# Kernel tuning notes

Hardware: AMD Instinct MI355X
Metric: run time of the kernel (lower is better)

The kernel has to match this reference:

```python
import jax, jax.numpy as jnp
import numpy as np

B, N, M = 8, 1024, 64          # graphs, ops/graph, machines/graph
OPF, MF = 16, 8                # raw feature dims
H, D, L = 8, 64, 3             # heads, head dim, HGT layers
F = H * D                      # 512 = hidden_dim * num_heads
KC = 8                         # compatible machines per op
NOP, NM = B * N, B * M
EPS = 1e-5


def _graph_ln(x, w, b):
    # PyG LayerNorm(mode='graph') with batch=None: scalar mean/std over the whole tensor
    x = x - x.mean()
    return x / (x.std() + EPS) * w + b


def _seg_softmax(a, idx, n):
    amax = jax.ops.segment_max(a, idx, num_segments=n)
    amax = jnp.where(jnp.isfinite(amax), amax, 0.0)
    ex = jnp.exp(a - amax[idx])
    s = jax.ops.segment_sum(ex, idx, num_segments=n)
    return ex / (s[idx] + 1e-16)


def _forward(op_x, machine_x, W_emb_op, b_emb_op, W_emb_m, b_emb_m,
             opn_w, opn_b, mn_w, mn_b, Wk, bk, Wq, bq, Wv, bv,
             A_rel, M_rel, p_rel, W_out, b_out, skip, ln_w, ln_b,
             ei_precedes, ei_canproc, ei_compat):
    x_op = _graph_ln(op_x @ W_emb_op + b_emb_op, opn_w, opn_b)
    x_m = _graph_ln(machine_x @ W_emb_m + b_emb_m, mn_w, mn_b)
    s0, d0 = ei_precedes   # op -> op
    s1, d1 = ei_canproc    # machine -> op
    s2, d2 = ei_compat     # op -> machine
    scale = 1.0 / jnp.sqrt(jnp.float32(D))
    for l in range(L):
        k_op = (x_op @ Wk[l, 0] + bk[l, 0]).reshape(NOP, H, D)
        q_op = (x_op @ Wq[l, 0] + bq[l, 0]).reshape(NOP, H, D)
        v_op = (x_op @ Wv[l, 0] + bv[l, 0]).reshape(NOP, H, D)
        k_m = (x_m @ Wk[l, 1] + bk[l, 1]).reshape(NM, H, D)
        q_m = (x_m @ Wq[l, 1] + bq[l, 1]).reshape(NM, H, D)
        v_m = (x_m @ Wv[l, 1] + bv[l, 1]).reshape(NM, H, D)
        # relation-specific per-head transforms (a_rel/m_rel of HGTConv)
        k0 = jnp.einsum('nhd,hde->nhe', k_op, A_rel[l, 0]); v0 = jnp.einsum('nhd,hde->nhe', v_op, M_rel[l, 0])
        k1 = jnp.einsum('nhd,hde->nhe', k_m, A_rel[l, 1]);  v1 = jnp.einsum('nhd,hde->nhe', v_m, M_rel[l, 1])
        k2 = jnp.einsum('nhd,hde->nhe', k_op, A_rel[l, 2]); v2 = jnp.einsum('nhd,hde->nhe', v_op, M_rel[l, 2])
        # attention into op nodes: joint softmax over both incoming edge types
        a0 = (q_op[d0] * k0[s0]).sum(-1) * p_rel[l, 0] * scale   # [E0,H]
        a1 = (q_op[d1] * k1[s1]).sum(-1) * p_rel[l, 1] * scale   # [E1,H]
        a_op = jnp.concatenate([a0, a1]); dd = jnp.concatenate([d0, d1])
        w = _seg_softmax(a_op, dd, NOP)
        msg = jnp.concatenate([v0[s0], v1[s1]]) * w[:, :, None]
        agg_op = jax.ops.segment_sum(msg, dd, num_segments=NOP).reshape(NOP, F)
        # attention into machine nodes
        a2 = (q_m[d2] * k2[s2]).sum(-1) * p_rel[l, 2] * scale
        w2 = _seg_softmax(a2, d2, NM)
        agg_m = jax.ops.segment_sum(v2[s2] * w2[:, :, None], d2, num_segments=NM).reshape(NM, F)
        # output projection + learned skip gate (HGTConv internals)
        o_op = jax.nn.gelu(agg_op, approximate=False) @ W_out[l, 0] + b_out[l, 0]
        o_m = jax.nn.gelu(agg_m, approximate=False) @ W_out[l, 1] + b_out[l, 1]
        g_op = jax.nn.sigmoid(skip[l, 0]); g_m = jax.nn.sigmoid(skip[l, 1])
        o_op = g_op * o_op + (1.0 - g_op) * x_op
        o_m = g_m * o_m + (1.0 - g_m) * x_m
        # wrapper residual + dropout(eval=identity) + graph layer norm
        x_op = _graph_ln(o_op + x_op, ln_w[l], ln_b[l])
        x_m = _graph_ln(o_m + x_m, ln_w[l], ln_b[l])
    fea_j = x_op.reshape(B, N, F)
    fea_m = x_m.reshape(B, M, F)
    return fea_j, fea_m, fea_j.mean(1, keepdims=True), fea_m.mean(1, keepdims=True)


def setup_inputs() -> dict:
    key = jax.random.key(0)
    ks = jax.random.split(key, 12)
    rng = np.random.default_rng(0)
    ids = np.arange(NOP).reshape(B, N)
    src0 = ids[:, :-1].ravel(); dst0 = ids[:, 1:].ravel()
    mach = rng.integers(0, M, size=(B, N, KC)) + (np.arange(B) * M)[:, None, None]
    ops = np.broadcast_to(ids[:, :, None], (B, N, KC))
    ei_precedes = jnp.asarray(np.stack([src0, dst0]), dtype=jnp.int32)
    ei_canproc = jnp.asarray(np.stack([mach.ravel(), ops.ravel()]), dtype=jnp.int32)
    ei_compat = jnp.asarray(np.stack([ops.ravel(), mach.ravel()]), dtype=jnp.int32)
    n = lambda k, sh, s=0.05: jax.random.normal(k, sh, dtype=jnp.float32) * s
    return dict(
        op_x=n(ks[0], (NOP, OPF), 1.0),
        machine_x=n(ks[1], (NM, MF), 1.0),
        W_emb_op=n(ks[2], (OPF, F)), b_emb_op=jnp.zeros((F,), jnp.float32),
        W_emb_m=n(ks[3], (MF, F)), b_emb_m=jnp.zeros((F,), jnp.float32),
        opn_w=jnp.ones((F,), jnp.float32), opn_b=jnp.zeros((F,), jnp.float32),
        mn_w=jnp.ones((F,), jnp.float32), mn_b=jnp.zeros((F,), jnp.float32),
        Wk=n(ks[4], (L, 2, F, F)), bk=jnp.zeros((L, 2, F), jnp.float32),
        Wq=n(ks[5], (L, 2, F, F)), bq=jnp.zeros((L, 2, F), jnp.float32),
        Wv=n(ks[6], (L, 2, F, F)), bv=jnp.zeros((L, 2, F), jnp.float32),
        A_rel=n(ks[7], (L, 3, H, D, D)), M_rel=n(ks[8], (L, 3, H, D, D)),
        p_rel=jnp.ones((L, 3, H), jnp.float32),
        W_out=n(ks[9], (L, 2, F, F)), b_out=jnp.zeros((L, 2, F), jnp.float32),
        skip=jnp.ones((L, 2), jnp.float32),
        ln_w=jnp.ones((L, F), jnp.float32), ln_b=jnp.zeros((L, F), jnp.float32),
        ei_precedes=ei_precedes, ei_canproc=ei_canproc, ei_compat=ei_compat,
    )


def reference(op_x, machine_x, W_emb_op, b_emb_op, W_emb_m, b_emb_m,
              opn_w, opn_b, mn_w, mn_b, Wk, bk, Wq, bq, Wv, bv,
              A_rel, M_rel, p_rel, W_out, b_out, skip, ln_w, ln_b,
              ei_precedes, ei_canproc, ei_compat):
    return _forward(op_x, machine_x, W_emb_op, b_emb_op, W_emb_m, b_emb_m,
                    opn_w, opn_b, mn_w, mn_b, Wk, bk, Wq, bq, Wv, bv,
                    A_rel, M_rel, p_rel, W_out, b_out, skip, ln_w, ln_b,
                    ei_precedes, ei_canproc, ei_compat)
```

## Files before the change

kernel.cpp:

```cpp
#include <hip/hip_runtime.h>

typedef unsigned short u16;
typedef __attribute__((ext_vector_type(4))) float floatx4;
typedef __attribute__((ext_vector_type(8))) short shortx8;
typedef __attribute__((ext_vector_type(4))) short shortx4;

#define NOPS 8192
#define NMS  512
#define CQ   2560
#define CM   1536
#define TOPC (NOPS*512)
#define TMC  (NMS*512)

__device__ __forceinline__ float bf2f(u16 u){ return __uint_as_float(((unsigned)u)<<16); }
__device__ __forceinline__ u16 f2bf(float f){
  unsigned u = __float_as_uint(f);
  u += 0x7FFFu + ((u>>16)&1u);
  return (u16)(u>>16);
}
__device__ __forceinline__ float wred(float v){
  #pragma unroll
  for (int o=32;o;o>>=1) v += __shfl_xor(v,o,64);
  return v;
}
__device__ __forceinline__ float geluf(float x){
  return 0.5f*x*(1.f+erff(x*0.70710678118654752f));
}
__device__ __forceinline__ void block_stat_out2(float s, float s2, float* pstat, int slot){
  __shared__ float sb[8];
  s = wred(s); s2 = wred(s2);
  int wv = threadIdx.x >> 6;
  if ((threadIdx.x & 63) == 0){ sb[wv*2] = s; sb[wv*2+1] = s2; }
  __syncthreads();
  if (threadIdx.x == 0){
    float a = 0.f, b = 0.f;
    int nw = blockDim.x >> 6;
    for (int i=0;i<nw;++i){ a += sb[i*2]; b += sb[i*2+1]; }
    pstat[slot*2]   = a;
    pstat[slot*2+1] = b;
  }
}

__global__ __launch_bounds__(256) void setup_all_k(
    const int* __restrict__ s1, float* __restrict__ Ct, float* __restrict__ Cn,
    const float* __restrict__ bq, float* bias_op, float* bias_m,
    const float* __restrict__ bk, const float* __restrict__ bv,
    const float* __restrict__ Ar, const float* __restrict__ Mr,
    const float* __restrict__ Wout, const float* __restrict__ Wq,
    u16* __restrict__ Wout_t, u16* __restrict__ Wc_op_t, u16* __restrict__ Wc_m_t,
    const float* __restrict__ Wk, const float* __restrict__ Wv,
    const float* __restrict__ Xop, const float* __restrict__ Wop, const float* __restrict__ bop,
    float* __restrict__ Yop, u16* __restrict__ Yop_bf,
    const float* __restrict__ Xm, const float* __restrict__ Wm, const float* __restrict__ bm_,
    float* __restrict__ Ym, u16* __restrict__ Ym_bf,
    float* pstat, float* pstat_m){
  __shared__ __align__(16) char smem[27648];
  int bid = blockIdx.x;
  int tid = threadIdx.x;
  if (bid < 1152){
    int eb = bid;
    const float *X, *W, *bias; float *Y, *ps; u16* Yb; int K, total4, nb, lb;
    if (eb < 1024){ X=Xop; W=Wop; bias=bop; Y=Yop; Yb=Yop_bf; ps=pstat;   K=16; total4=TOPC/4; nb=1024; lb=eb; }
    else          { X=Xm;  W=Wm;  bias=bm_; Y=Ym;  Yb=Ym_bf;  ps=pstat_m; K=8;  total4=TMC/4;  nb=128;  lb=eb-1024; }
    float s = 0.f, s2 = 0.f;
    for (int idx = lb*256 + tid; idx < total4; idx += nb*256){
      int n = idx >> 7, f4 = idx & 127;
      floatx4 v = *(const floatx4*)(bias + f4*4);
      const float* xrow = X + n*K;
      for (int c=0;c<K;++c){
        float xc = xrow[c];
        floatx4 wv = *(const floatx4*)(W + c*512 + f4*4);
        #pragma unroll
        for (int e=0;e<4;++e) v[e] += xc*wv[e];
      }
      shortx4 sv;
      #pragma unroll
      for (int e=0;e<4;++e){ sv[e] = (short)f2bf(v[e]); s += v[e]; s2 += v[e]*v[e]; }
      *(floatx4*)(Y + (size_t)idx*4) = v;
      *(shortx4*)(Yb + (size_t)idx*4) = sv;
    }
    block_stat_out2(s, s2, ps, lb);
  } else if (bid < 1920){
    u16 (*t)[65] = (u16(*)[65])smem;
    int id2 = bid - 1152;
    int g = id2 >> 6; int rem = id2 & 63;
    int kb = (rem >> 3) * 64, nb = (rem & 7) * 64;
    const float* s; u16* d;
    if (g < 6){
      s = Wout + (size_t)g*262144;
      d = Wout_t + (size_t)g*262144;
    } else {
      int blk = g - 6; int l = blk >> 1, side = blk & 1;
      s = Wq + (size_t)blk*262144;
      d = side ? (Wc_m_t + (size_t)l*CM*512) : (Wc_op_t + (size_t)l*CQ*512);
    }
    int tx = tid & 63, ty4 = tid >> 6;
    #pragma unroll 4
    for (int p=0;p<16;++p){
      int k = ty4 + p*4;
      t[k][tx] = f2bf(s[(size_t)(kb+k)*512 + nb + tx]);
    }
    __syncthreads();
    #pragma unroll 4
    for (int p=0;p<16;++p){
      int n = ty4 + p*4;
      d[(size_t)(nb+n)*512 + kb + tx] = t[tx][n];
    }
  } else if (bid < 2496){
    u16* As = (u16*)smem;
    u16* Bs = As + 64*72;
    int id3 = bid - 1920;
    int gx = id3 >> 2;
    int cc0 = (id3 & 3) * 128;
    int l = gx/48; int rem = gx - l*48; int s = rem >> 3; int h = rem & 7;
    int side = (s < 4) ? 0 : 1;
    int r = (s < 4) ? (s+1) : (s-3);
    int useK = side==0 ? (s==0 || s==2) : (s==4);
    int rel  = side==0 ? ((s<2)?0:2) : 1;
    const float* W   = (useK ? Wk : Wv) + (size_t)(l*2+side)*262144;
    const float* Rel = (useK ? Ar : Mr) + ((size_t)(l*3+rel)*8 + h)*4096;
    int h64 = h*64;
    u16* Wt = side ? (Wc_m_t + (size_t)l*CM*512) : (Wc_op_t + (size_t)l*CQ*512);
    int rbase = r*512 + h64;
    int lane = tid & 63, wave = tid >> 6;
    {
      int d = tid >> 2, e0 = (tid & 3) * 16;
      #pragma unroll
      for (int j=0;j<16;++j) As[(e0+j)*72 + d] = f2bf(Rel[d*64 + e0 + j]);
    }
    {
      int ccl = tid >> 1, d0 = (tid & 1) * 32;
      const float* src = W + (size_t)(cc0+ccl)*512 + h64 + d0;
      #pragma unroll
      for (int j=0;j<32;j+=4){
        floatx4 v = *(const floatx4*)(src + j);
        shortx4 sv;
        #pragma unroll
        for (int e=0;e<4;++e) sv[e] = (short)f2bf(v[e]);
        *(shortx4*)(Bs + ccl*72 + d0 + j) = sv;
      }
    }
    __syncthreads();
    int wm = wave & 1, wn = wave >> 1;
    int mrow = lane & 15, quad = lane >> 4;
    floatx4 acc[2][4];
    #pragma unroll
    for (int a=0;a<2;++a)
      #pragma unroll
      for (int b=0;b<4;++b) acc[a][b] = (floatx4){0.f,0.f,0.f,0.f};
    #pragma unroll
    for (int ks=0; ks<2; ++ks){
      shortx8 af[2], bf[4];
      #pragma unroll
      for (int mt=0;mt<2;++mt) af[mt] = *(const shortx8*)(As + (wm*32 + mt*16 + mrow)*72 + ks*32 + quad*8);
      #pragma unroll
      for (int nt=0;nt<4;++nt) bf[nt] = *(const shortx8*)(Bs + (wn*64 + nt*16 + mrow)*72 + ks*32 + quad*8);
      #pragma unroll
      for (int mt=0;mt<2;++mt)
        #pragma unroll
        for (int nt=0;nt<4;++nt)
          acc[mt][nt] = __builtin_amdgcn_mfma_f32_16x16x32_bf16(af[mt], bf[nt], acc[mt][nt], 0, 0, 0);
    }
    #pragma unroll
    for (int mt=0;mt<2;++mt){
      #pragma unroll
      for (int nt=0;nt<4;++nt){
        int ccl = wn*64 + nt*16 + mrow;
        #pragma unroll
        for (int r2=0;r2<4;++r2){
          int e = wm*32 + mt*16 + quad*4 + r2;
          Wt[(size_t)(rbase + e)*512 + cc0 + ccl] = f2bf(acc[mt][nt][r2]);
        }
      }
    }
  } else if (bid < 4544){
    int idx = (bid-2496)*256 + tid;
    int n = idx >> 6, l = idx & 63;
    const int* row = s1 + n*8;
    int cnt = 0;
    #pragma unroll
    for (int j=0;j<8;++j) cnt += ((row[j] & 63) == l);
    float f = (float)cnt;
    Cn[(size_t)n*64 + l] = f;
    int b = n >> 10, nl = n & 1023;
    Ct[(size_t)((b<<6) + l)*1024 + nl] = f;
  } else if (bid < 4556){
    int i = (bid-4544)*256 + tid;
    int l = i >> 10, side = (i >> 9) & 1, f = i & 511;
    float v = bq[(l*2+side)*512 + f];
    if (side==0) bias_op[l*CQ + f] = v; else bias_m[l*CM + f] = v;
  } else {
    if (tid >= 64) return;
    int gx = bid - 4556; int e = tid;
    int l = gx/48; int rem = gx - l*48; int s = rem >> 3; int h = rem & 7;
    int side = (s < 4) ? 0 : 1;
    int r = (s < 4) ? (s+1) : (s-3);
    int useK = side==0 ? (s==0 || s==2) : (s==4);
    int rel  = side==0 ? ((s<2)?0:2) : 1;
    const float* bb  = (useK ? bk : bv) + (size_t)(l*2+side)*512 + h*64;
    const float* Rel = (useK ? Ar : Mr) + ((size_t)(l*3+rel)*8 + h)*4096;
    float acc = 0.f;
    for (int d=0; d<64; ++d) acc += bb[d]*Rel[d*64 + e];
    float* bias = side ? (bias_m + l*CM) : (bias_op + l*CQ);
    bias[r*512 + h*64 + e] = acc;
  }
}

__global__ __launch_bounds__(256) void foldk(u16* __restrict__ Wc_op_t, u16* __restrict__ Wc_m_t,
                                             float* __restrict__ bias_op, float* __restrict__ bias_m,
                                             float* __restrict__ u_op, float* __restrict__ u_m,
                                             const float* __restrict__ opn_w, const float* __restrict__ opn_b,
                                             const float* __restrict__ mn_w, const float* __restrict__ mn_b,
                                             const float* __restrict__ ln_w, const float* __restrict__ ln_b){
  int bid = blockIdx.x, tid = threadIdx.x;
  int rloc = tid >> 2, t = tid & 3;
  int side, l; u16* Wt; float* bias; float* u;
  if (bid < 120){
    int row = bid*64 + rloc; side = 0; l = row/2560; int j = row - l*2560;
    Wt = Wc_op_t + ((size_t)l*CQ + j)*512; bias = bias_op + l*CQ + j; u = u_op + l*CQ + j;
  } else {
    int row = (bid-120)*64 + rloc; side = 1; l = row/1536; int j = row - l*1536;
    Wt = Wc_m_t + ((size_t)l*CM + j)*512; bias = bias_m + l*CM + j; u = u_m + l*CM + j;
  }
  const float* w = side ? (l==0 ? mn_w : ln_w + (l-1)*512) : (l==0 ? opn_w : ln_w + (l-1)*512);
  const float* b = side ? (l==0 ? mn_b : ln_b + (l-1)*512) : (l==0 ? opn_b : ln_b + (l-1)*512);
  float up = 0.f, vp = 0.f;
  for (int k = t*128; k < t*128 + 128; k += 8){
    shortx8 wv = *(shortx8*)(Wt + k);
    #pragma unroll
    for (int e=0;e<8;++e){
      float x = bf2f((u16)wv[e]);
      float wk = w[k+e];
      up += wk*x; vp += b[k+e]*x;
      wv[e] = (short)f2bf(x*wk);
    }
    *(shortx8*)(Wt + k) = wv;
  }
  up += __shfl_xor(up,1,64); up += __shfl_xor(up,2,64);
  vp += __shfl_xor(vp,1,64); vp += __shfl_xor(vp,2,64);
  if (t == 0){ *u = up; *bias += vp; }
}

__global__ __launch_bounds__(256) void ln2_k(const float* __restrict__ src_op, float* __restrict__ dst_op,
                                             const float* __restrict__ w_op, const float* __restrict__ b_op,
                                             const float* __restrict__ src_m, float* __restrict__ dst_m,
                                             const float* __restrict__ w_m, const float* __restrict__ b_m,
                                             const float* __restrict__ pstat, const float* __restrict__ pstat_m,
                                             int nbo, int nbm){
  int bid = blockIdx.x;
  const float *src, *w, *b, *ps; float* dst; int total4, nb, lb, nblk; float inv_n;
  if (bid < 1024){ src=src_op; dst=dst_op; w=w_op; b=b_op; ps=pstat;
                   total4=TOPC/4; nb=1024; lb=bid; nblk=nbo; inv_n=1.f/TOPC; }
  else           { src=src_m;  dst=dst_m;  w=w_m;  b=b_m;  ps=pstat_m;
                   total4=TMC/4;  nb=128;  lb=bid-1024; nblk=nbm; inv_n=1.f/TMC; }
  __shared__ float sb[8];
  __shared__ float mr[2];
  float s = 0.f, s2 = 0.f;
  for (int i = threadIdx.x; i < nblk; i += 256){ s += ps[2*i]; s2 += ps[2*i+1]; }
  s = wred(s); s2 = wred(s2);
  int wv = threadIdx.x >> 6;
  if ((threadIdx.x & 63) == 0){ sb[wv*2] = s; sb[wv*2+1] = s2; }
  __syncthreads();
  if (threadIdx.x == 0){
    float a = 0.f, bsum = 0.f;
    for (int i=0;i<4;++i){ a += sb[i*2]; bsum += sb[i*2+1]; }
    float mean = a * inv_n;
    float var  = fmaxf(bsum * inv_n - mean*mean, 0.f);
    mr[0] = mean;
    mr[1] = 1.f/(sqrtf(var) + 1e-5f);
  }
  __syncthreads();
  float mean = mr[0], rinv = mr[1];
  const floatx4* s4 = (const floatx4*)src;
  floatx4* d4 = (floatx4*)dst;
  const floatx4* w4 = (const floatx4*)w;
  const floatx4* b4 = (const floatx4*)b;
  for (int i = lb*256 + threadIdx.x; i < total4; i += nb*256){
    int f = i & 127;
    floatx4 v = s4[i], wv2 = w4[f], bv = b4[f];
    #pragma unroll
    for (int e=0;e<4;++e) v[e] = (v[e]-mean)*rinv*wv2[e] + bv[e];
    d4[i] = v;
  }
}

__device__ __forceinline__ void gemm_gate_core(u16* As, u16* Bs, float* stb,
                                               const u16* __restrict__ A, const u16* __restrict__ Bt,
                                               const float* __restrict__ xr, const float* __restrict__ bo,
                                               const float* __restrict__ sk,
                                               const float* __restrict__ lnw, const float* __restrict__ lnb,
                                               const float* __restrict__ psr, int np, float inv_n,
                                               float* __restrict__ Y, u16* __restrict__ Ybf,
                                               float* pstat, int slot, int bx, int by){
  const int tid = threadIdx.x;
  const int lane = tid & 63, wave = tid >> 6;
  {
    float s = 0.f, s2 = 0.f;
    for (int i = tid; i < np; i += 256){ s += psr[2*i]; s2 += psr[2*i+1]; }
    s = wred(s); s2 = wred(s2);
    if (lane == 0){ stb[wave*2] = s; stb[wave*2+1] = s2; }
    __syncthreads();
    if (tid == 0){
      float a = 0.f, bb = 0.f;
      for (int i=0;i<4;++i){ a += stb[2*i]; bb += stb[2*i+1]; }
      float mean = a * inv_n;
      float var = fmaxf(bb * inv_n - mean*mean, 0.f);
      stb[8] = mean;
      stb[9] = 1.f/(sqrtf(var) + 1e-5f);
    }
    __syncthreads();
  }
  const float mean = stb[8], rinv = stb[9];
  const int bm = by * 128, bn = bx * 128;
  const int wm = wave & 1, wn = wave >> 1;
  const int mrow = lane & 15, quad = lane >> 4;
  const u16* Ab = A + (size_t)bm*512;
  const u16* Bb = Bt + (size_t)bn*512;
  floatx4 acc[4][4];
  #pragma unroll
  for (int a=0;a<4;++a)
    #pragma unroll
    for (int b=0;b<4;++b) acc[a][b] = (floatx4){0.f,0.f,0.f,0.f};
  const int r0 = tid >> 2, c0 = (tid & 3) * 8;
  const int r1 = (tid+256) >> 2, c1 = ((tid+256) & 3) * 8;
  const int lds0 = wave*512;
  const int lds1 = wave*512 + 2048;
  for (int k0 = 0; k0 < 512; k0 += 32){
    __builtin_amdgcn_global_load_lds((const __attribute__((address_space(1))) void*)(Ab + (size_t)r0*512 + k0 + c0),
                                     (__attribute__((address_space(3))) void*)(As + lds0), 16, 0, 0);
    __builtin_amdgcn_global_load_lds((const __attribute__((address_space(1))) void*)(Ab + (size_t)r1*512 + k0 + c1),
                                     (__attribute__((address_space(3))) void*)(As + lds1), 16, 0, 0);
    __builtin_amdgcn_global_load_lds((const __attribute__((address_space(1))) void*)(Bb + (size_t)r0*512 + k0 + c0),
                                     (__attribute__((address_space(3))) void*)(Bs + lds0), 16, 0, 0);
    __builtin_amdgcn_global_load_lds((const __attribute__((address_space(1))) void*)(Bb + (size_t)r1*512 + k0 + c1),
                                     (__attribute__((address_space(3))) void*)(Bs + lds1), 16, 0, 0);
    __syncthreads();
    shortx8 af[4], bf[4];
    #pragma unroll
    for (int mt=0;mt<4;++mt) af[mt] = *(const shortx8*)(As + (wm*64 + mt*16 + mrow)*32 + quad*8);
    #pragma unroll
    for (int nt=0;nt<4;++nt) bf[nt] = *(const shortx8*)(Bs + (wn*64 + nt*16 + mrow)*32 + quad*8);
    #pragma unroll
    for (int mt=0;mt<4;++mt)
      #pragma unroll
      for (int nt=0;nt<4;++nt)
        acc[mt][nt] = __builtin_amdgcn_mfma_f32_16x16x32_bf16(af[mt], bf[nt], acc[mt][nt], 0, 0, 0);
    __syncthreads();
  }
  float g = 1.f/(1.f+expf(-(*sk)));
  float s = 0.f, s2 = 0.f;
  #pragma unroll
  for (int mt=0;mt<4;++mt){
    #pragma unroll
    for (int nt=0;nt<4;++nt){
      int col = bn + wn*64 + nt*16 + mrow;
      float bval = bo[col];
      float lw = lnw[col]*rinv, lb = lnb[col];
      #pragma unroll
      for (int r2=0;r2<4;++r2){
        int row = bm + wm*64 + mt*16 + quad*4 + r2;
        float v = acc[mt][nt][r2] + bval;
        float xv = (xr[(size_t)row*512 + col] - mean)*lw + lb;
        float o = g*v + (2.f-g)*xv;
        Y[(size_t)row*512 + col] = o;
        Ybf[(size_t)row*512 + col] = f2bf(o);
        s += o; s2 += o*o;
      }
    }
  }
  block_stat_out2(s, s2, pstat, slot);
}
__global__ __launch_bounds__(256) void gemmgate2_k(
    const u16* A1, const u16* B1, const float* x1, const float* bo1, const float* sk1,
    const float* lnw1, const float* lnb1, float* Y1, u16* Yb1, float* ps1w, int nblk1,
    const u16* A2, const u16* B2, const float* x2, const float* bo2, const float* sk2,
    const float* lnw2, const float* lnb2, float* Y2, u16* Yb2, float* ps2w,
    const float* ps1r, int np1, const float* ps2r, int np2){
  __shared__ u16 As[128*32];
  __shared__ u16 Bs[128*32];
  __shared__ float stb[12];
  int id = blockIdx.x;
  if (id < nblk1)
    gemm_gate_core(As, Bs, stb, A1, B1, x1, bo1, sk1, lnw1, lnb1, ps1r, np1, 1.f/TOPC,
                   Y1, Yb1, ps1w, id, id % 4, id / 4);
  else {
    int j = id - nblk1;
    gemm_gate_core(As, Bs, stb, A2, B2, x2, bo2, sk2, lnw2, lnb2, ps2r, np2, 1.f/TMC,
                   Y2, Yb2, ps2w, j, j % 4, j / 4);
  }
}

__device__ __forceinline__ void stage_half8(const u16* __restrict__ src, int kc, u16* region, int tid){
  int wave = tid >> 6;
  #pragma unroll
  for (int j=0;j<2;++j){
    int idx = j*512 + tid;
    int row = idx >> 2, qp2 = idx & 3;
    int qs = qp2 ^ (((row >> 3) & 1) << 1);
    __builtin_amdgcn_global_load_lds(
      (const __attribute__((address_space(1))) void*)(src + (size_t)row*512 + kc + qs*8),
      (__attribute__((address_space(3))) void*)(region + (j*512 + wave*64)*8),
      16, 0, 0);
  }
}

#define MFMA_QUAD(MH) do { \
  __builtin_amdgcn_s_barrier(); \
  asm volatile("s_waitcnt lgkmcnt(0)" ::: "memory"); \
  __builtin_amdgcn_sched_barrier(0); \
  __builtin_amdgcn_s_setprio(1); \
  _Pragma("unroll") \
  for (int mt=0;mt<4;++mt){ \
    _Pragma("unroll") \
    for (int nt=0;nt<4;++nt) \
      acc[(MH)*4+mt][nt] = __builtin_amdgcn_mfma_f32_16x16x32_bf16(af[mt], bf[nt], acc[(MH)*4+mt][nt], 0, 0, 0); \
  } \
  __builtin_amdgcn_s_setprio(0); \
} while(0)

__global__ __launch_bounds__(512, 2) void gemm8_k(
    const u16* __restrict__ A1, const u16* __restrict__ B1, const float* __restrict__ bias1,
    const float* __restrict__ u1, u16* __restrict__ C1, int N1, int nbx1, int nblk1,
    const u16* __restrict__ A2, const u16* __restrict__ B2, const float* __restrict__ bias2p,
    const float* __restrict__ u2, u16* __restrict__ C2, int N2, int nbx2,
    const float* __restrict__ ps1, int np1, const float* __restrict__ ps2, int np2){
  extern __shared__ u16 lds[];
  float* statsh = (float*)(lds + 65536);
  int id = blockIdx.x;
  const u16 *A, *Bt; const float *bias, *uvec, *ps; u16* C; int N, bx, by, np; float inv_n;
  if (id < nblk1){
    int xcd = id & 7, loc = id >> 3;
    int wg = xcd * (nblk1 >> 3) + loc;
    A=A1; Bt=B1; bias=bias1; uvec=u1; C=C1; N=N1; bx=wg%nbx1; by=wg/nbx1;
    ps=ps1; np=np1; inv_n=1.f/TOPC;
  }
  else { int j=id-nblk1; A=A2; Bt=B2; bias=bias2p; uvec=u2; C=C2; N=N2; bx=j%nbx2; by=j/nbx2;
    ps=ps2; np=np2; inv_n=1.f/TMC; }
  const int tid = threadIdx.x, lane = tid & 63, wave = tid >> 6;
  {
    float s = 0.f, s2 = 0.f;
    for (int i = tid; i < np; i += 512){ s += ps[2*i]; s2 += ps[2*i+1]; }
    s = wred(s); s2 = wred(s2);
    if (lane == 0){ statsh[wave*2] = s; statsh[wave*2+1] = s2; }
    __syncthreads();
    if (tid == 0){
      float a = 0.f, bb = 0.f;
      for (int i=0;i<8;++i){ a += statsh[2*i]; bb += statsh[2*i+1]; }
      float mean = a * inv_n;
      float var = fmaxf(bb * inv_n - mean*mean, 0.f);
      statsh[16] = mean;
      statsh[17] = 1.f/(sqrtf(var) + 1e-5f);
    }
    __syncthreads();
  }
  const float mean = statsh[16], rinv = statsh[17];
  const int wm = wave & 1, wn = wave >> 1;
  const int mrow = lane & 15, quad = lane >> 4;
  const int qp = quad ^ ((mrow & 8) ? 2 : 0);
  const u16* Ab = A + (size_t)(by*256)*512;
  const u16* Bb = Bt + (size_t)(bx*256)*512;

  floatx4 acc[8][4];
  #pragma unroll
  for (int a=0;a<8;++a)
    #pragma unroll
    for (int b=0;b<4;++b) acc[a][b] = (floatx4){0.f,0.f,0.f,0.f};

  stage_half8(Ab, 0,  lds,          tid);
  stage_half8(Bb, 0,  lds + 16384,  tid);
  stage_half8(Ab, 32, lds + 8192,   tid);
  stage_half8(Bb, 32, lds + 24576,  tid);
  stage_half8(Ab, 64, lds + 32768,  tid);
  stage_half8(Bb, 64, lds + 49152,  tid);
  asm volatile("s_waitcnt vmcnt(8)" ::: "memory");
  __builtin_amdgcn_s_barrier();

  for (int t = 0; t < 8; ++t){
    const int s = t & 1;
    u16* Sbase = lds + s*32768;
    u16* Obase = lds + (s^1)*32768;
    const u16* a0 = Sbase + (wm*128 + mrow)*32 + qp*8;
    const u16* b0 = Sbase + 16384 + (wn*64 + mrow)*32 + qp*8;
    const int kc1 = ((t < 7) ? (t+1) : 7)*64 + 32;
    const int kc2 = ((t < 6) ? (t+2) : 7)*64;
    shortx8 af[4], bf[4];

    #pragma unroll
    for (int mt=0;mt<4;++mt) af[mt] = *(const shortx8*)(a0 + mt*512);
    #pragma unroll
    for (int nt=0;nt<4;++nt) bf[nt] = *(const shortx8*)(b0 + nt*512);
    stage_half8(Ab, kc1, Obase + 8192, tid);
    MFMA_QUAD(0);
    __builtin_amdgcn_s_barrier();

    #pragma unroll
    for (int mt=0;mt<4;++mt) af[mt] = *(const shortx8*)(a0 + 2048 + mt*512);
    stage_half8(Bb, kc1, Obase + 24576, tid);
    MFMA_QUAD(1);
    asm volatile("s_waitcnt vmcnt(8)" ::: "memory");
    __builtin_amdgcn_s_barrier();

    #pragma unroll
    for (int mt=0;mt<4;++mt) af[mt] = *(const shortx8*)(a0 + 8192 + mt*512);
    #pragma unroll
    for (int nt=0;nt<4;++nt) bf[nt] = *(const shortx8*)(b0 + 8192 + nt*512);
    stage_half8(Ab, kc2, Sbase, tid);
    MFMA_QUAD(0);
    __builtin_amdgcn_s_barrier();

    #pragma unroll
    for (int mt=0;mt<4;++mt) af[mt] = *(const shortx8*)(a0 + 8192 + 2048 + mt*512);
    stage_half8(Bb, kc2, Sbase + 16384, tid);
    MFMA_QUAD(1);
    asm volatile("s_waitcnt vmcnt(8)" ::: "memory");
    __builtin_amdgcn_s_barrier();
  }

  const float rm = rinv*mean;
  const int crow0 = by*256 + wm*128 + quad*4;
  const int ccol0 = bx*256 + wn*64 + mrow;
  float bv[4], uv[4];
  #pragma unroll
  for (int nt=0;nt<4;++nt){
    int col = ccol0 + nt*16;
    bv[nt] = bias[col];
    uv[nt] = uvec[col];
  }
  #pragma unroll
  for (int mh=0;mh<2;++mh){
    #pragma unroll
    for (int mt=0;mt<4;++mt){
      int row = crow0 + mh*64 + mt*16;
      #pragma unroll
      for (int nt=0;nt<4;++nt){
        int col = ccol0 + nt*16;
        #pragma unroll
        for (int r2=0;r2<4;++r2)
          C[(size_t)(row+r2)*N + col] = f2bf(rinv*acc[mh*4+mt][nt][r2] + bv[nt] - rm*uv[nt]);
      }
    }
  }
}

__global__ __launch_bounds__(256) void attn_k(const u16* __restrict__ qkv_op, const u16* __restrict__ qkv_m,
                                              const float* __restrict__ prel, const float* __restrict__ Cn,
                                              const float* __restrict__ Ct,
                                              u16* __restrict__ agg_op, u16* __restrict__ agg_m){
  __shared__ __align__(16) char smem[37376];
  int id = blockIdx.x;
  int tid = threadIdx.x, lane = tid & 63, wave = tid >> 6;
  int mrow = lane & 15, quad = lane >> 4;
  if (id < 256){
    u16* qs  = (u16*)smem;
    u16* ks  = (u16*)(smem + 2304);
    u16* vsT = (u16*)(smem + 11520);
    u16* Ps  = (u16*)(smem + 20736);
    float (*redv)[4][16] = (float(*)[4][16])(smem + 23040);
    int g = id & 3; int bh = id >> 2; int b = bh >> 3, h = bh & 7;
    int w = wave;
    float p2 = prel[16 + h] * 0.125f;
    if (tid < 128){
      int r = tid >> 3, cg = (tid & 7) * 8;
      *(shortx8*)(qs + r*72 + cg) = *(const shortx8*)(qkv_m + (size_t)(b*64 + g*16 + r)*CM + h*64 + cg);
    }
    const float* ctbase = Ct + (size_t)(b*64 + g*16 + mrow)*1024;
    float mold_m = -1e30f;
    float mold4[4] = {-1e30f,-1e30f,-1e30f,-1e30f};
    float L = 0.f;
    floatx4 O = (floatx4){0,0,0,0};
    for (int ch = 0; ch < 16; ++ch){
      int nb = ch*64;
      #pragma unroll
      for (int i=0;i<2;++i){
        int idx = i*256 + tid;
        int r = idx >> 3, cg = (idx & 7) * 8;
        *(shortx8*)(ks + r*72 + cg) =
          *(const shortx8*)(qkv_op + (size_t)(b*1024 + nb + r)*CQ + 1536 + h*64 + cg);
        shortx8 vv = *(const shortx8*)(qkv_op + (size_t)(b*1024 + nb + r)*CQ + 2048 + h*64 + cg);
        #pragma unroll
        for (int e=0;e<8;++e) vsT[(cg+e)*72 + r] = (u16)vv[e];
      }
      __syncthreads();
      floatx4 sa, cv;
      {
        floatx4 acc = (floatx4){0,0,0,0};
        #pragma unroll
        for (int kk=0; kk<2; ++kk){
          shortx8 af = *(const shortx8*)(ks + (w*16 + mrow)*72 + kk*32 + quad*8);
          shortx8 bf = *(const shortx8*)(qs + mrow*72 + kk*32 + quad*8);
          acc = __builtin_amdgcn_mfma_f32_16x16x32_bf16(af, bf, acc, 0, 0, 0);
        }
        int nloc = w*16 + quad*4;
        cv = *(const floatx4*)(ctbase + nb + nloc);
        #pragma unroll
        for (int r2=0;r2<4;++r2) acc[r2] *= p2;
        sa = acc;
      }
      float cm = -1e30f;
      #pragma unroll
      for (int r2=0;r2<4;++r2)
        if (cv[r2] > 0.f) cm = fmaxf(cm, sa[r2]);
      cm = fmaxf(cm, __shfl_xor(cm, 16, 64));
      cm = fmaxf(cm, __shfl_xor(cm, 32, 64));
      if (lane < 16) redv[0][w][lane] = cm;
      __syncthreads();
      float mnew_m = fmaxf(fmaxf(redv[0][0][mrow], redv[0][1][mrow]),
                           fmaxf(redv[0][2][mrow], redv[0][3][mrow]));
      mnew_m = fmaxf(mnew_m, mold_m);
      float sL = expf(mold_m - mnew_m);
      mold_m = mnew_m;
      float sO[4];
      #pragma unroll
      for (int r2=0;r2<4;++r2){
        int r = quad*4 + r2;
        float mn = fmaxf(fmaxf(redv[0][0][r], redv[0][1][r]),
                         fmaxf(redv[0][2][r], redv[0][3][r]));
        mn = fmaxf(mn, mold4[r2]);
        sO[r2] = expf(mold4[r2] - mn);
        mold4[r2] = mn;
      }
      float Lsum = 0.f;
      {
        int nloc = w*16 + quad*4;
        shortx4 pv;
        #pragma unroll
        for (int r2=0;r2<4;++r2){
          float e = (cv[r2] > 0.f) ? cv[r2]*expf(sa[r2] - mnew_m) : 0.f;
          Lsum += e;
          pv[r2] = (short)f2bf(e);
        }
        *(shortx4*)(Ps + mrow*72 + nloc) = pv;
      }
      L = L*sL + Lsum;
      __syncthreads();
      #pragma unroll
      for (int r2=0;r2<4;++r2) O[r2] *= sO[r2];
      #pragma unroll
      for (int kk=0; kk<2; ++kk){
        shortx8 af = *(const shortx8*)(Ps + mrow*72 + kk*32 + quad*8);
        shortx8 bf = *(const shortx8*)(vsT + (w*16 + mrow)*72 + kk*32 + quad*8);
        O = __builtin_amdgcn_mfma_f32_16x16x32_bf16(af, bf, O, 0, 0, 0);
      }
      __syncthreads();
    }
    L += __shfl_xor(L, 16, 64);
    L += __shfl_xor(L, 32, 64);
    if (lane < 16) redv[1][w][lane] = L;
    __syncthreads();
    #pragma unroll
    for (int r2=0;r2<4;++r2){
      int m = quad*4 + r2;
      float Ls = redv[1][0][m] + redv[1][1][m] + redv[1][2][m] + redv[1][3][m];
      float v = O[r2] / (Ls + 1e-16f);
      agg_m[(size_t)(b*64 + g*16 + m)*512 + h*64 + w*16 + mrow] = f2bf(geluf(v));
    }
  } else {
    u16* smem16 = (u16*)smem;
    u16* As = smem16;
    u16* Bs = smem16 + 4608;
    float* Sbuf = (float*)smem;
    u16* P   = smem16 + 9216;
    u16* v1T = smem16 + 13824;
    float* wpreS = (float*)(smem + 36864);
    float* linvS = (float*)(smem + 37120);
    int id2 = id - 256;
    int bh = id2 >> 4; int b = bh >> 3, h = bh & 7;
    int n0 = (id2 & 15) * 64;
    int wm = wave & 1, wn = wave >> 1;
    int srow = tid >> 2, scol = (tid & 3) * 16;
    float p1 = prel[8 + h] * 0.125f;
    {
      const u16* src = qkv_op + (size_t)(b*1024 + n0 + srow)*CQ + h*64 + scol;
      *(shortx8*)(As + srow*72 + scol)     = *(const shortx8*)(src);
      *(shortx8*)(As + srow*72 + scol + 8) = *(const shortx8*)(src + 8);
    }
    {
      const u16* src = qkv_m + (size_t)(b*64 + srow)*CM + 512 + h*64 + scol;
      *(shortx8*)(Bs + srow*72 + scol)     = *(const shortx8*)(src);
      *(shortx8*)(Bs + srow*72 + scol + 8) = *(const shortx8*)(src + 8);
    }
    {
      const u16* src = qkv_m + (size_t)(b*64 + srow)*CM + 1024 + h*64 + scol;
      shortx8 v0 = *(const shortx8*)(src);
      shortx8 v1 = *(const shortx8*)(src + 8);
      #pragma unroll
      for (int e=0;e<8;++e){ v1T[(scol+e)*72 + srow] = (u16)v0[e]; v1T[(scol+8+e)*72 + srow] = (u16)v1[e]; }
    }
    __syncthreads();
    floatx4 acc[2][2];
    #pragma unroll
    for (int a=0;a<2;++a){ acc[a][0] = (floatx4){0,0,0,0}; acc[a][1] = (floatx4){0,0,0,0}; }
    #pragma unroll
    for (int ks=0; ks<2; ++ks){
      shortx8 af[2], bf[2];
      #pragma unroll
      for (int mt=0;mt<2;++mt) af[mt] = *(const shortx8*)(As + (wm*32 + mt*16 + mrow)*72 + ks*32 + quad*8);
      #pragma unroll
      for (int nt=0;nt<2;++nt) bf[nt] = *(const shortx8*)(Bs + (wn*32 + nt*16 + mrow)*72 + ks*32 + quad*8);
      #pragma unroll
      for (int mt=0;mt<2;++mt)
        #pragma unroll
        for (int nt=0;nt<2;++nt)
          acc[mt][nt] = __builtin_amdgcn_mfma_f32_16x16x32_bf16(af[mt], bf[nt], acc[mt][nt], 0, 0, 0);
    }
    __syncthreads();
    #pragma unroll
    for (int mt=0;mt<2;++mt){
      #pragma unroll
      for (int nt=0;nt<2;++nt){
        int m = wn*32 + nt*16 + mrow;
        #pragma unroll
        for (int r2=0;r2<4;++r2){
          int nl = wm*32 + mt*16 + quad*4 + r2;
          Sbuf[nl*66 + m] = acc[mt][nt][r2] * p1;
        }
      }
    }
    __syncthreads();
    {
      int row = srow;
      int mb  = scol;
      int n_g = b*1024 + n0 + row;
      int nl  = n0 + row;
      float sp = -1e30f;
      if (nl > 0){
        float p0 = prel[h] * 0.125f;
        const u16* qp = qkv_op + (size_t)n_g*CQ + h*64 + mb;
        const u16* kp = qkv_op + (size_t)(n_g-1)*CQ + 512 + h*64 + mb;
        shortx8 qa = *(const shortx8*)(qp), qb2 = *(const shortx8*)(qp + 8);
        shortx8 ka = *(const shortx8*)(kp), kb2 = *(const shortx8*)(kp + 8);
        float d = 0.f;
        #pragma unroll
        for (int e=0;e<8;++e) d += bf2f((u16)qa[e])*bf2f((u16)ka[e]) + bf2f((u16)qb2[e])*bf2f((u16)kb2[e]);
        d += __shfl_xor(d, 1, 64);
        d += __shfl_xor(d, 2, 64);
        sp = d * p0;
      }
      const float* crow = Cn + (size_t)n_g*64 + mb;
      float cv[16];
      float mx = sp;
      #pragma unroll
      for (int j=0;j<16;++j){
        cv[j] = crow[j];
        if (cv[j] > 0.f) mx = fmaxf(mx, Sbuf[row*66 + mb + j]);
      }
      mx = fmaxf(mx, __shfl_xor(mx, 1, 64));
      mx = fmaxf(mx, __shfl_xor(mx, 2, 64));
      float L = 0.f;
      #pragma unroll
      for (int j=0;j<16;j+=4){
        shortx4 pv;
        #pragma unroll
        for (int e=0;e<4;++e){
          float w = (cv[j+e] > 0.f) ? cv[j+e]*expf(Sbuf[row*66 + mb + j + e] - mx) : 0.f;
          L += w;
          pv[e] = (short)f2bf(w);
        }
        *(shortx4*)(P + row*72 + mb + j) = pv;
      }
      L += __shfl_xor(L, 1, 64);
      L += __shfl_xor(L, 2, 64);
      float ep = (nl > 0) ? expf(sp - mx) : 0.f;
      L += ep;
      if ((tid & 3) == 0){ wpreS[row] = ep; linvS[row] = 1.f/(L + 1e-16f); }
    }
    __syncthreads();
    floatx4 po[2][2];
    #pragma unroll
    for (int a=0;a<2;++a){ po[a][0] = (floatx4){0,0,0,0}; po[a][1] = (floatx4){0,0,0,0}; }
    #pragma unroll
    for (int ks=0; ks<2; ++ks){
      shortx8 paf[2], pbf[2];
      #pragma unroll
      for (int mt=0;mt<2;++mt) paf[mt] = *(const shortx8*)(P + (wm*32 + mt*16 + mrow)*72 + ks*32 + quad*8);
      #pragma unroll
      for (int nt=0;nt<2;++nt) pbf[nt] = *(const shortx8*)(v1T + (wn*32 + nt*16 + mrow)*72 + ks*32 + quad*8);
      #pragma unroll
      for (int mt=0;mt<2;++mt)
        #pragma unroll
        for (int nt=0;nt<2;++nt)
          po[mt][nt] = __builtin_amdgcn_mfma_f32_16x16x32_bf16(paf[mt], pbf[nt], po[mt][nt], 0, 0, 0);
    }
    #pragma unroll
    for (int mt=0;mt<2;++mt){
      #pragma unroll
      for (int nt=0;nt<2;++nt){
        int d = wn*32 + nt*16 + mrow;
        #pragma unroll
        for (int r2=0;r2<4;++r2){
          int rl = wm*32 + mt*16 + quad*4 + r2;
          int n = n0 + rl;
          size_t ng = (size_t)b*1024 + n;
          float v = po[mt][nt][r2];
          if (n > 0) v += wpreS[rl] * bf2f(qkv_op[(ng-1)*CQ + 1024 + h*64 + d]);
          v *= linvS[rl];
          agg_op[ng*512 + h*64 + d] = f2bf(geluf(v));
        }
      }
    }
  }
}

__global__ __launch_bounds__(512) void meanj_part_k(const float* __restrict__ xo, float* scratchJ){
  int b = blockIdx.x, chunk = blockIdx.y, f = threadIdx.x;
  float s = 0.f;
  for (int r=0;r<128;++r){
    int row = b*1024 + chunk*128 + r;
    s += xo[(size_t)row*512 + f];
  }
  scratchJ[(b*8 + chunk)*512 + f] = s;
}
__global__ __launch_bounds__(512) void mean2_k(const float* __restrict__ scratchJ, float* __restrict__ out){
  int i = blockIdx.x*512 + threadIdx.x;
  if (i < 4096){
    int b = i >> 9, f = i & 511;
    float s = 0.f;
    #pragma unroll
    for (int c=0;c<8;++c) s += scratchJ[(b*8+c)*512 + f];
    out[4456448 + i] = s * (1.f/1024.f);
  } else {
    int j = i - 4096;
    int b = j >> 9, f = j & 511;
    float s = 0.f;
    for (int r=0;r<64;++r) s += out[(size_t)TOPC + (size_t)(b*64+r)*512 + f];
    out[4460544 + j] = s * (1.f/64.f);
  }
}

extern "C" void kernel_launch(void* const* d_in, const int* in_sizes, int n_in,
                              void* d_out, int out_size, void* d_ws, size_t ws_size,
                              hipStream_t stream){
  const float* op_x      = (const float*)d_in[0];
  const float* machine_x = (const float*)d_in[1];
  const float* W_emb_op  = (const float*)d_in[2];
  const float* b_emb_op  = (const float*)d_in[3];
  const float* W_emb_m   = (const float*)d_in[4];
  const float* b_emb_m   = (const float*)d_in[5];
  const float* opn_w     = (const float*)d_in[6];
  const float* opn_b     = (const float*)d_in[7];
  const float* mn_w      = (const float*)d_in[8];
  const float* mn_b      = (const float*)d_in[9];
  const float* Wk        = (const float*)d_in[10];
  const float* bk        = (const float*)d_in[11];
  const float* Wq        = (const float*)d_in[12];
  const float* bq        = (const float*)d_in[13];
  const float* Wv        = (const float*)d_in[14];
  const float* bv        = (const float*)d_in[15];
  const float* A_rel     = (const float*)d_in[16];
  const float* M_rel     = (const float*)d_in[17];
  const float* p_rel     = (const float*)d_in[18];
  const float* W_out     = (const float*)d_in[19];
  const float* b_out     = (const float*)d_in[20];
  const float* skip      = (const float*)d_in[21];
  const float* ln_w      = (const float*)d_in[22];
  const float* ln_b      = (const float*)d_in[23];
  const int* s1          = (const int*)d_in[25];
  float* out = (float*)d_out;

  char* ws = (char*)d_ws;
  size_t off = 0;
  auto alloc = [&](size_t bytes)->void*{
    void* p = ws + off;
    off = (off + bytes + 255) & ~(size_t)255;
    return p;
  };
  float* pstat     = (float*)alloc(8192*4);
  float* scratchJ  = (float*)alloc(32768*4);
  float* Ct        = (float*)alloc((size_t)NMS*1024*4);
  float* Cn        = (float*)alloc((size_t)NOPS*64*4);
  float* x_op      = (float*)alloc((size_t)NOPS*512*4);
  u16*   x_op_bf   = (u16*)  alloc((size_t)NOPS*512*2);
  float* x_m       = (float*)alloc((size_t)NMS*512*4);
  u16*   x_m_bf    = (u16*)  alloc((size_t)NMS*512*2);
  u16*   qkv_op    = (u16*)  alloc((size_t)NOPS*CQ*2);
  u16*   qkv_m     = (u16*)  alloc((size_t)NMS*CM*2);
  u16*   agg_op    = (u16*)  alloc((size_t)NOPS*512*2);
  u16*   agg_m     = (u16*)  alloc((size_t)NMS*512*2);
  u16*   Wc_op_t   = (u16*)  alloc((size_t)3*CQ*512*2);
  float* bias_op   = (float*)alloc((size_t)3*CQ*4);
  u16*   Wc_m_t    = (u16*)  alloc((size_t)3*CM*512*2);
  float* bias_m    = (float*)alloc((size_t)3*CM*4);
  float* u_op      = (float*)alloc((size_t)3*CQ*4);
  float* u_m       = (float*)alloc((size_t)3*CM*4);
  u16*   Wout_t    = (u16*)  alloc((size_t)6*262144*2);
  float* psA   = pstat;          float* psA_m = pstat + 2048;
  float* psB   = pstat + 4096;   float* psB_m = pstat + 6144;

  setup_all_k<<<4700,256,0,stream>>>(s1, Ct, Cn, bq, bias_op, bias_m, bk, bv, A_rel, M_rel,
                                     W_out, Wq, Wout_t, Wc_op_t, Wc_m_t, Wk, Wv,
                                     op_x, W_emb_op, b_emb_op, x_op, x_op_bf,
                                     machine_x, W_emb_m, b_emb_m, x_m, x_m_bf, psA, psA_m);
  foldk<<<192,256,0,stream>>>(Wc_op_t, Wc_m_t, bias_op, bias_m, u_op, u_m,
                              opn_w, opn_b, mn_w, mn_b, ln_w, ln_b);

  for (int l=0; l<3; ++l){
    float *psR, *psR_m, *psW, *psW_m; int npo, npm;
    if (l == 0){ psR=psA; psR_m=psA_m; psW=psB; psW_m=psB_m; npo=1024; npm=128; }
    else if (l == 1){ psR=psB; psR_m=psB_m; psW=psA; psW_m=psA_m; npo=256; npm=16; }
    else { psR=psA; psR_m=psA_m; psW=psB; psW_m=psB_m; npo=256; npm=16; }
    const float* lnw_o = (l==0) ? opn_w : ln_w + (l-1)*512;
    const float* lnb_o = (l==0) ? opn_b : ln_b + (l-1)*512;
    const float* lnw_m2 = (l==0) ? mn_w : ln_w + (l-1)*512;
    const float* lnb_m2 = (l==0) ? mn_b : ln_b + (l-1)*512;
    gemm8_k<<<332,512,131136,stream>>>(x_op_bf, Wc_op_t + (size_t)l*CQ*512, bias_op + l*CQ, u_op + l*CQ,
                                       qkv_op, CQ, 10, 320,
                                       x_m_bf, Wc_m_t + (size_t)l*CM*512, bias_m + l*CM, u_m + l*CM,
                                       qkv_m, CM, 6,
                                       psR, npo, psR_m, npm);
    attn_k<<<1280,256,0,stream>>>(qkv_op, qkv_m, p_rel + l*24, Cn, Ct, agg_op, agg_m);
    gemmgate2_k<<<272,256,0,stream>>>(agg_op, Wout_t + (size_t)(l*2+0)*262144, x_op,
                                      b_out + (size_t)(l*2+0)*512, skip + l*2+0,
                                      lnw_o, lnb_o, x_op, x_op_bf, psW, 256,
                                      agg_m, Wout_t + (size_t)(l*2+1)*262144, x_m,
                                      b_out + (size_t)(l*2+1)*512, skip + l*2+1,
                                      lnw_m2, lnb_m2, x_m, x_m_bf, psW_m,
                                      psR, npo, psR_m, npm);
  }

  ln2_k<<<1152,256,0,stream>>>(x_op, out, ln_w + 1024, ln_b + 1024,
                               x_m, out + TOPC, ln_w + 1024, ln_b + 1024,
                               psB, psB_m, 256, 16);

  meanj_part_k<<<dim3(8,8),512,0,stream>>>(out, scratchJ);
  mean2_k<<<16,512,0,stream>>>(scratchJ, out);
}
```

Baseline: 505.4 us.

## Simplify QKV GEMM to double-buffered K=32 pipeline with half the LDS

Replaces the three-stage, 64-wide-K staging schedule in the fused QKV GEMM with a plain two-buffer ping-pong over 32-wide K slices. Each iteration prefetches the next slice, runs two MFMA quads, then fully drains the loads with vmcnt(0) before a barrier. This halves dynamic LDS so two blocks can share a CU, and the launch bound is raised to request higher occupancy. The costs are a full wait on loads every iteration, which gives less latency hiding than before. The higher occupancy request also tightens the register budget against the large accumulator array, which risks spills.

```diff
diff --git a/kernel.cpp b/kernel.cpp
--- a/kernel.cpp
+++ b/kernel.cpp
@@ -404,28 +404,14 @@
   }
 }
 
-#define MFMA_QUAD(MH) do { \
-  __builtin_amdgcn_s_barrier(); \
-  asm volatile("s_waitcnt lgkmcnt(0)" ::: "memory"); \
-  __builtin_amdgcn_sched_barrier(0); \
-  __builtin_amdgcn_s_setprio(1); \
-  _Pragma("unroll") \
-  for (int mt=0;mt<4;++mt){ \
-    _Pragma("unroll") \
-    for (int nt=0;nt<4;++nt) \
-      acc[(MH)*4+mt][nt] = __builtin_amdgcn_mfma_f32_16x16x32_bf16(af[mt], bf[nt], acc[(MH)*4+mt][nt], 0, 0, 0); \
-  } \
-  __builtin_amdgcn_s_setprio(0); \
-} while(0)
-
-__global__ __launch_bounds__(512, 2) void gemm8_k(
+__global__ __launch_bounds__(512, 4) void gemm8_k(
     const u16* __restrict__ A1, const u16* __restrict__ B1, const float* __restrict__ bias1,
     const float* __restrict__ u1, u16* __restrict__ C1, int N1, int nbx1, int nblk1,
     const u16* __restrict__ A2, const u16* __restrict__ B2, const float* __restrict__ bias2p,
     const float* __restrict__ u2, u16* __restrict__ C2, int N2, int nbx2,
     const float* __restrict__ ps1, int np1, const float* __restrict__ ps2, int np2){
   extern __shared__ u16 lds[];
-  float* statsh = (float*)(lds + 65536);
+  float* statsh = (float*)(lds + 32768);
   int id = blockIdx.x;
   const u16 *A, *Bt; const float *bias, *uvec, *ps; u16* C; int N, bx, by, np; float inv_n;
   if (id < nblk1){
@@ -466,53 +452,46 @@
     #pragma unroll
     for (int b=0;b<4;++b) acc[a][b] = (floatx4){0.f,0.f,0.f,0.f};
 
-  stage_half8(Ab, 0,  lds,          tid);
-  stage_half8(Bb, 0,  lds + 16384,  tid);
-  stage_half8(Ab, 32, lds + 8192,   tid);
-  stage_half8(Bb, 32, lds + 24576,  tid);
-  stage_half8(Ab, 64, lds + 32768,  tid);
-  stage_half8(Bb, 64, lds + 49152,  tid);
-  asm volatile("s_waitcnt vmcnt(8)" ::: "memory");
+  stage_half8(Ab, 0, lds,        tid);
+  stage_half8(Bb, 0, lds + 8192, tid);
+  asm volatile("s_waitcnt vmcnt(0)" ::: "memory");
   __builtin_amdgcn_s_barrier();
 
-  for (int t = 0; t < 8; ++t){
+  for (int t = 0; t < 16; ++t){
     const int s = t & 1;
-    u16* Sbase = lds + s*32768;
-    u16* Obase = lds + (s^1)*32768;
+    u16* Sbase = lds + s*16384;
+    u16* Obase = lds + (s^1)*16384;
+    const int kcn = ((t < 15) ? (t+1) : 15) * 32;
+    stage_half8(Ab, kcn, Obase,        tid);
+    stage_half8(Bb, kcn, Obase + 8192, tid);
     const u16* a0 = Sbase + (wm*128 + mrow)*32 + qp*8;
-    const u16* b0 = Sbase + 16384 + (wn*64 + mrow)*32 + qp*8;
-    const int kc1 = ((t < 7) ? (t+1) : 7)*64 + 32;
-    const int kc2 = ((t < 6) ? (t+2) : 7)*64;
+    const u16* b0 = Sbase + 8192 + (wn*64 + mrow)*32 + qp*8;
     shortx8 af[4], bf[4];
-
     #pragma unroll
     for (int mt=0;mt<4;++mt) af[mt] = *(const shortx8*)(a0 + mt*512);
     #pragma unroll
     for (int nt=0;nt<4;++nt) bf[nt] = *(const shortx8*)(b0 + nt*512);
-    stage_half8(Ab, kc1, Obase + 8192, tid);
-    MFMA_QUAD(0);
-    __builtin_amdgcn_s_barrier();
-
+    asm volatile("s_waitcnt lgkmcnt(0)" ::: "memory");
+    __builtin_amdgcn_sched_barrier(0);
+    __builtin_amdgcn_s_setprio(1);
+    #pragma unroll
+    for (int mt=0;mt<4;++mt)
+      #pragma unroll
+      for (int nt=0;nt<4;++nt)
+        acc[mt][nt] = __builtin_amdgcn_mfma_f32_16x16x32_bf16(af[mt], bf[nt], acc[mt][nt], 0, 0, 0);
+    __builtin_amdgcn_s_setprio(0);
     #pragma unroll
     for (int mt=0;mt<4;++mt) af[mt] = *(const shortx8*)(a0 + 2048 + mt*512);
-    stage_half8(Bb, kc1, Obase + 24576, tid);
-    MFMA_QUAD(1);
-    asm volatile("s_waitcnt vmcnt(8)" ::: "memory");
-    __builtin_amdgcn_s_barrier();
-
-    #pragma unroll
-    for (int mt=0;mt<4;++mt) af[mt] = *(const shortx8*)(a0 + 8192 + mt*512);
-    #pragma unroll
-    for (int nt=0;nt<4;++nt) bf[nt] = *(const shortx8*)(b0 + 8192 + nt*512);
-    stage_half8(Ab, kc2, Sbase, tid);
-    MFMA_QUAD(0);
-    __builtin_amdgcn_s_barrier();
-
-    #pragma unroll
-    for (int mt=0;mt<4;++mt) af[mt] = *(const shortx8*)(a0 + 8192 + 2048 + mt*512);
-    stage_half8(Bb, kc2, Sbase + 16384, tid);
-    MFMA_QUAD(1);
-    asm volatile("s_waitcnt vmcnt(8)" ::: "memory");
+    asm volatile("s_waitcnt lgkmcnt(0)" ::: "memory");
+    __builtin_amdgcn_sched_barrier(0);
+    __builtin_amdgcn_s_setprio(1);
+    #pragma unroll
+    for (int mt=0;mt<4;++mt)
+      #pragma unroll
+      for (int nt=0;nt<4;++nt)
+        acc[4+mt][nt] = __builtin_amdgcn_mfma_f32_16x16x32_bf16(af[mt], bf[nt], acc[4+mt][nt], 0, 0, 0);
+    __builtin_amdgcn_s_setprio(0);
+    asm volatile("s_waitcnt vmcnt(0)" ::: "memory");
     __builtin_amdgcn_s_barrier();
   }
 
@@ -902,11 +881,11 @@
     const float* lnb_o = (l==0) ? opn_b : ln_b + (l-1)*512;
     const float* lnw_m2 = (l==0) ? mn_w : ln_w + (l-1)*512;
     const float* lnb_m2 = (l==0) ? mn_b : ln_b + (l-1)*512;
-    gemm8_k<<<332,512,131136,stream>>>(x_op_bf, Wc_op_t + (size_t)l*CQ*512, bias_op + l*CQ, u_op + l*CQ,
-                                       qkv_op, CQ, 10, 320,
-                                       x_m_bf, Wc_m_t + (size_t)l*CM*512, bias_m + l*CM, u_m + l*CM,
-                                       qkv_m, CM, 6,
-                                       psR, npo, psR_m, npm);
+    gemm8_k<<<332,512,65600,stream>>>(x_op_bf, Wc_op_t + (size_t)l*CQ*512, bias_op + l*CQ, u_op + l*CQ,
+                                      qkv_op, CQ, 10, 320,
+                                      x_m_bf, Wc_m_t + (size_t)l*CM*512, bias_m + l*CM, u_m + l*CM,
+                                      qkv_m, CM, 6,
+                                      psR, npo, psR_m, npm);
     attn_k<<<1280,256,0,stream>>>(qkv_op, qkv_m, p_rel + l*24, Cn, Ct, agg_op, agg_m);
     gemmgate2_k<<<272,256,0,stream>>>(agg_op, Wout_t + (size_t)(l*2+0)*262144, x_op,
                                       b_out + (size_t)(l*2+0)*512, skip + l*2+0,
```

After: 1.011 ms. 2x slower.
